# Kernel tuning notes

Hardware: AMD Instinct MI355X
Metric: run time of the kernel (lower is better)

## Reference

```python
import jax, jax.numpy as jnp
import numpy as np

BSZ, NGEN, NCLS, SEQ, G = 64, 128, 30, 2048, 16  # G = gold triples per example (fixed)

POS_NAMES = ["sub_start_logits", "sub_end_logits", "obj_start_logits", "obj_end_logits",
             "aspect_start_logits", "aspect_end_logits", "opinion_start_logits", "opinion_end_logits"]
GOLD_NAMES = ["gold_sub_start", "gold_sub_end", "gold_obj_start", "gold_obj_end",
              "gold_aspect_start", "gold_aspect_end", "gold_opinion_start", "gold_opinion_end"]


def _lsa(C):
    """Exact rectangular linear sum assignment (Jonker-Volgenant shortest augmenting
    path), equivalent to scipy.optimize.linear_sum_assignment. Returns (row_ind, col_ind)."""
    C = np.asarray(C, dtype=np.float64)
    transposed = C.shape[0] > C.shape[1]
    if transposed:
        C = C.T
    n, m = C.shape
    u = np.zeros(n + 1)
    v = np.zeros(m + 1)
    p = np.zeros(m + 1, dtype=np.int64)    # p[j] = row (1-based) assigned to column j
    way = np.zeros(m + 1, dtype=np.int64)
    for i in range(1, n + 1):
        p[0] = i
        j0 = 0
        minv = np.full(m + 1, np.inf)
        used = np.zeros(m + 1, dtype=bool)
        while True:
            used[j0] = True
            i0 = p[j0]
            cur = C[i0 - 1] - u[i0] - v[1:]
            better = (~used[1:]) & (cur < minv[1:])
            minv[1:] = np.where(better, cur, minv[1:])
            way[1:] = np.where(better, j0, way[1:])
            cand = np.where(~used[1:], minv[1:], np.inf)
            j1 = int(np.argmin(cand)) + 1
            delta = cand[j1 - 1]
            for j in np.where(used)[0]:
                u[p[j]] += delta
                v[j] -= delta
            minv[~used] -= delta
            j0 = j1
            if p[j0] == 0:
                break
        while j0:
            j1 = way[j0]
            p[j0] = p[j1]
            j0 = j1
    col = np.full(n, -1, dtype=np.int64)
    for j in range(1, m + 1):
        if p[j]:
            col[p[j] - 1] = j - 1
    row = np.arange(n, dtype=np.int64)
    if transposed:
        order = np.argsort(col)
        return col[order], row[order]
    return row, col


def setup_inputs() -> dict:
    key = jax.random.key(0)
    ks = jax.random.split(key, 18)
    d = {"pred_rel_logits": jax.random.normal(ks[0], (BSZ, NGEN, NCLS), jnp.float32)}
    for i, name in enumerate(POS_NAMES):
        d[name] = jax.random.normal(ks[1 + i], (BSZ, NGEN, SEQ), jnp.float32)
    d["gold_rel"] = jax.random.randint(ks[9], (BSZ * G,), 0, NCLS)
    for i, name in enumerate(GOLD_NAMES):
        d[name] = jax.random.randint(ks[10 + i], (BSZ * G,), 0, SEQ)
    return d


def _cost(pred_rel_logits, sub_start_logits, sub_end_logits, obj_start_logits, obj_end_logits,
          aspect_start_logits, aspect_end_logits, opinion_start_logits, opinion_end_logits,
          gold_rel, gold_sub_start, gold_sub_end, gold_obj_start, gold_obj_end,
          gold_aspect_start, gold_aspect_end, gold_opinion_start, gold_opinion_end):
    bsz, ngen = pred_rel_logits.shape[:2]
    sm = lambda x: jax.nn.softmax(x.reshape(bsz * ngen, -1), axis=-1)
    # cost: [bsz*ngen, total_gold], matcher == 'avg'
    cost = -(sm(pred_rel_logits)[:, gold_rel]
             + sm(sub_start_logits)[:, gold_sub_start] + sm(sub_end_logits)[:, gold_sub_end]
             + sm(obj_start_logits)[:, gold_obj_start] + sm(obj_end_logits)[:, gold_obj_end]
             + sm(aspect_start_logits)[:, gold_aspect_start] + sm(aspect_end_logits)[:, gold_aspect_end]
             + sm(opinion_start_logits)[:, gold_opinion_start] + sm(opinion_end_logits)[:, gold_opinion_end])
    return cost.reshape(bsz, ngen, -1)


_cost_jit = jax.jit(_cost)


def reference(pred_rel_logits, sub_start_logits, sub_end_logits, obj_start_logits, obj_end_logits,
              aspect_start_logits, aspect_end_logits, opinion_start_logits, opinion_end_logits,
              gold_rel, gold_sub_start, gold_sub_end, gold_obj_start, gold_obj_end,
              gold_aspect_start, gold_aspect_end, gold_opinion_start, gold_opinion_end):
    cost = _cost_jit(pred_rel_logits, sub_start_logits, sub_end_logits, obj_start_logits,
                     obj_end_logits, aspect_start_logits, aspect_end_logits,
                     opinion_start_logits, opinion_end_logits,
                     gold_rel, gold_sub_start, gold_sub_end, gold_obj_start, gold_obj_end,
                     gold_aspect_start, gold_aspect_end, gold_opinion_start, gold_opinion_end)
    cnp = np.asarray(cost)
    rows = np.zeros((BSZ, G), dtype=np.int64)
    cols = np.zeros((BSZ, G), dtype=np.int64)
    # per-example assignment on the example's own block of gold columns (mirrors cost.split)
    for b in range(BSZ):
        r, c = _lsa(cnp[b, :, b * G:(b + 1) * G])
        rows[b], cols[b] = r, c
    return cost, jnp.asarray(rows), jnp.asarray(cols)
```

## Files before the change

### kernel.cpp

```cpp
#include <hip/hip_runtime.h>
#include <math.h>

#define BSZ   64
#define NGEN  128
#define NCLS  30
#define SEQ   2048
#define G     16
#define NQ    (BSZ * NGEN)
#define TG    (BSZ * G)
#define COST_ELEMS ((size_t)NQ * TG)
#define OFF_ROWS COST_ELEMS
#define OFF_COLS (COST_ELEMS + TG)

__global__ __launch_bounds__(256) void cost_kernel(
    const float* __restrict__ rel,
    const float* __restrict__ p0, const float* __restrict__ p1,
    const float* __restrict__ p2, const float* __restrict__ p3,
    const float* __restrict__ p4, const float* __restrict__ p5,
    const float* __restrict__ p6, const float* __restrict__ p7,
    const int* __restrict__ grel,
    const int* __restrict__ g0, const int* __restrict__ g1,
    const int* __restrict__ g2, const int* __restrict__ g3,
    const int* __restrict__ g4, const int* __restrict__ g5,
    const int* __restrict__ g6, const int* __restrict__ g7,
    float* __restrict__ out)
{
    __shared__ float ex[4][SEQ];
    __shared__ float relex[32];

    const int q    = blockIdx.x;
    const int tid  = threadIdx.x;
    const int wave = tid >> 6;
    const int lane = tid & 63;

    float acc[4] = {0.f, 0.f, 0.f, 0.f};

    #pragma unroll
    for (int phase = 0; phase < 2; ++phase) {
        const float* pk;
        if      (wave == 0) pk = (phase == 0) ? p0 : p4;
        else if (wave == 1) pk = (phase == 0) ? p1 : p5;
        else if (wave == 2) pk = (phase == 0) ? p2 : p6;
        else                pk = (phase == 0) ? p3 : p7;

        const float4* row4 = (const float4*)(pk + (size_t)q * SEQ);
        float4 x[8];
        float mx = -INFINITY;
        #pragma unroll
        for (int j = 0; j < 8; ++j) {
            x[j] = row4[lane + 64 * j];
            mx = fmaxf(mx, fmaxf(fmaxf(x[j].x, x[j].y), fmaxf(x[j].z, x[j].w)));
        }
        #pragma unroll
        for (int off = 32; off; off >>= 1) mx = fmaxf(mx, __shfl_xor(mx, off));

        float s = 0.f;
        #pragma unroll
        for (int j = 0; j < 8; ++j) {
            x[j].x = __expf(x[j].x - mx); x[j].y = __expf(x[j].y - mx);
            x[j].z = __expf(x[j].z - mx); x[j].w = __expf(x[j].w - mx);
            s += (x[j].x + x[j].y) + (x[j].z + x[j].w);
        }
        #pragma unroll
        for (int off = 32; off; off >>= 1) s += __shfl_xor(s, off);
        const float r = 1.f / s;

        float4* exw = (float4*)ex[wave];
        #pragma unroll
        for (int j = 0; j < 8; ++j) {
            float4 e = x[j];
            e.x *= r; e.y *= r; e.z *= r; e.w *= r;
            exw[lane + 64 * j] = e;
        }

        if (phase == 0 && wave == 0) {
            float xv = (lane < NCLS) ? rel[(size_t)q * NCLS + lane] : -INFINITY;
            float m2 = xv;
            #pragma unroll
            for (int off = 32; off; off >>= 1) m2 = fmaxf(m2, __shfl_xor(m2, off));
            float e2 = (lane < NCLS) ? __expf(xv - m2) : 0.f;
            float s2 = e2;
            #pragma unroll
            for (int off = 32; off; off >>= 1) s2 += __shfl_xor(s2, off);
            float r2 = 1.f / s2;
            if (lane < 32) relex[lane] = (lane < NCLS) ? e2 * r2 : 0.f;
        }
        __syncthreads();

        const int* __restrict__ gA = phase ? g4 : g0;
        const int* __restrict__ gB = phase ? g5 : g1;
        const int* __restrict__ gC = phase ? g6 : g2;
        const int* __restrict__ gD = phase ? g7 : g3;
        #pragma unroll
        for (int c = 0; c < 4; ++c) {
            const int t = tid + 256 * c;
            acc[c] += ex[0][gA[t]];
            acc[c] += ex[1][gB[t]];
            acc[c] += ex[2][gC[t]];
            acc[c] += ex[3][gD[t]];
            if (phase == 1) acc[c] += relex[grel[t]];
        }
        __syncthreads();
    }

    #pragma unroll
    for (int c = 0; c < 4; ++c) {
        const int t = tid + 256 * c;
        out[(size_t)q * TG + t] = -acc[c];
    }
}

__global__ __launch_bounds__(64) void lsa_kernel(const float* __restrict__ cost,
                                                 float* __restrict__ out)
{
    const int b   = blockIdx.x;
    const int tid = threadIdx.x;

    __shared__ float  C[G][NGEN];
    __shared__ double u[G + 1], v[NGEN + 1], minv[NGEN + 1];
    __shared__ int    p[NGEN + 1], way[NGEN + 1], used[NGEN + 1];
    __shared__ int    colArr[G];

    for (int e = tid; e < G * NGEN; e += 64) {
        int j = e >> 4, i = e & (G - 1);
        C[i][j] = cost[((size_t)(b * NGEN + j)) * TG + b * G + i];
    }
    for (int e = tid; e <= NGEN; e += 64) { v[e] = 0.0; p[e] = 0; }
    if (tid <= G) u[tid] = 0.0;
    __syncthreads();

    const double INFD = 1e300;

    for (int i = 1; i <= G; ++i) {
        if (tid == 0) { p[0] = i; used[0] = 0; }
        #pragma unroll
        for (int c = 0; c < 2; ++c) {
            int j = 1 + tid + 64 * c;
            minv[j] = INFD; used[j] = 0;
        }
        __syncthreads();

        int j0 = 0;
        while (true) {
            if (tid == 0) used[j0] = 1;
            __syncthreads();

            const int    i0  = p[j0];
            const double ui0 = u[i0];

            double bv = INFD; int bj = NGEN + 1;
            #pragma unroll
            for (int c = 0; c < 2; ++c) {
                int j = 1 + tid + 64 * c;
                if (!used[j]) {
                    double cur = (double)C[i0 - 1][j - 1] - ui0 - v[j];
                    if (cur < minv[j]) { minv[j] = cur; way[j] = j0; }
                    double cd = minv[j];
                    if (cd < bv) { bv = cd; bj = j; }
                }
            }
            #pragma unroll
            for (int off = 32; off; off >>= 1) {
                double ov = __shfl_xor(bv, off);
                int    oj = __shfl_xor(bj, off);
                if (ov < bv || (ov == bv && oj < bj)) { bv = ov; bj = oj; }
            }
            const double delta = bv;
            const int    j1    = bj;
            __syncthreads();

            #pragma unroll
            for (int c = 0; c < 2; ++c) {
                int j = 1 + tid + 64 * c;
                if (used[j]) { u[p[j]] += delta; v[j] -= delta; }
                else         { minv[j] -= delta; }
            }
            if (tid == 0) u[p[0]] += delta;
            __syncthreads();

            j0 = j1;
            if (p[j0] == 0) break;
        }

        while (j0) {
            int j1a = way[j0];
            if (tid == 0) p[j0] = p[j1a];
            __syncthreads();
            j0 = j1a;
        }
        __syncthreads();
    }

    #pragma unroll
    for (int c = 0; c < 2; ++c) {
        int j = 1 + tid + 64 * c;
        int pi = p[j];
        if (pi != 0) colArr[pi - 1] = j - 1;
    }
    __syncthreads();
    if (tid < G) {
        int ci = colArr[tid];
        int rank = 0;
        #pragma unroll
        for (int j = 0; j < G; ++j) rank += (colArr[j] < ci) ? 1 : 0;
        out[OFF_ROWS + b * G + rank] = (float)ci;
        out[OFF_COLS + b * G + rank] = (float)tid;
    }
}

extern "C" void kernel_launch(void* const* d_in, const int* in_sizes, int n_in,
                              void* d_out, int out_size, void* d_ws, size_t ws_size,
                              hipStream_t stream) {
    const float* rel = (const float*)d_in[0];
    const float* p0  = (const float*)d_in[1];
    const float* p1  = (const float*)d_in[2];
    const float* p2  = (const float*)d_in[3];
    const float* p3  = (const float*)d_in[4];
    const float* p4  = (const float*)d_in[5];
    const float* p5  = (const float*)d_in[6];
    const float* p6  = (const float*)d_in[7];
    const float* p7  = (const float*)d_in[8];
    const int* grel = (const int*)d_in[9];
    const int* g0 = (const int*)d_in[10];
    const int* g1 = (const int*)d_in[11];
    const int* g2 = (const int*)d_in[12];
    const int* g3 = (const int*)d_in[13];
    const int* g4 = (const int*)d_in[14];
    const int* g5 = (const int*)d_in[15];
    const int* g6 = (const int*)d_in[16];
    const int* g7 = (const int*)d_in[17];
    float* out = (float*)d_out;

    cost_kernel<<<NQ, 256, 0, stream>>>(rel, p0, p1, p2, p3, p4, p5, p6, p7,
                                        grel, g0, g1, g2, g3, g4, g5, g6, g7, out);
    lsa_kernel<<<BSZ, 64, 0, stream>>>(out, out);
}
```

Before: 505.7 us.

## Widen cost blocks to 1024 threads, drop max-subtraction, register-resident single-wave LSA

The cost kernel now uses 1024 threads per query, with four waves per softmax row. It drops the max subtraction from the softmax, folds normalization into an FMA on the gather, and preloads gold indices into registers. The LSA kernel keeps u, v, minv, way, used and p in per-lane registers and communicates through wave shuffles, which removes all shared-memory barriers from the Hungarian inner loop. Skipping the max subtraction risks exp overflow on large logits. The 1024-thread blocks with 32KB of LDS may also limit occupancy.

```diff
diff --git a/kernel.cpp b/kernel.cpp
--- a/kernel.cpp
+++ b/kernel.cpp
@@ -12,7 +12,7 @@
 #define OFF_ROWS COST_ELEMS
 #define OFF_COLS (COST_ELEMS + TG)
 
-__global__ __launch_bounds__(256) void cost_kernel(
+__global__ __launch_bounds__(1024, 8) void cost_kernel(
     const float* __restrict__ rel,
     const float* __restrict__ p0, const float* __restrict__ p1,
     const float* __restrict__ p2, const float* __restrict__ p3,
@@ -27,138 +27,139 @@
 {
     __shared__ float ex[4][SEQ];
     __shared__ float relex[32];
-
+    __shared__ float spart[16];
+    __shared__ float srel;
+
+    const int tid  = threadIdx.x;
     const int q    = blockIdx.x;
-    const int tid  = threadIdx.x;
-    const int wave = tid >> 6;
     const int lane = tid & 63;
-
-    float acc[4] = {0.f, 0.f, 0.f, 0.f};
+    const int wv   = tid >> 6;
+    const int kloc = tid >> 8;
+    const int r    = tid & 255;
+
+    const int j0_ = g0[tid], j1_ = g1[tid], j2_ = g2[tid], j3_ = g3[tid];
+    const int j4_ = g4[tid], j5_ = g5[tid], j6_ = g6[tid], j7_ = g7[tid];
+    const int jr_ = grel[tid];
+
+    float acc = 0.f;
 
     #pragma unroll
     for (int phase = 0; phase < 2; ++phase) {
-        const float* pk;
-        if      (wave == 0) pk = (phase == 0) ? p0 : p4;
-        else if (wave == 1) pk = (phase == 0) ? p1 : p5;
-        else if (wave == 2) pk = (phase == 0) ? p2 : p6;
-        else                pk = (phase == 0) ? p3 : p7;
+        const float* pk =
+            (kloc == 0) ? (phase ? p4 : p0) :
+            (kloc == 1) ? (phase ? p5 : p1) :
+            (kloc == 2) ? (phase ? p6 : p2) :
+                          (phase ? p7 : p3);
 
         const float4* row4 = (const float4*)(pk + (size_t)q * SEQ);
-        float4 x[8];
-        float mx = -INFINITY;
-        #pragma unroll
-        for (int j = 0; j < 8; ++j) {
-            x[j] = row4[lane + 64 * j];
-            mx = fmaxf(mx, fmaxf(fmaxf(x[j].x, x[j].y), fmaxf(x[j].z, x[j].w)));
-        }
-        #pragma unroll
-        for (int off = 32; off; off >>= 1) mx = fmaxf(mx, __shfl_xor(mx, off));
-
-        float s = 0.f;
-        #pragma unroll
-        for (int j = 0; j < 8; ++j) {
-            x[j].x = __expf(x[j].x - mx); x[j].y = __expf(x[j].y - mx);
-            x[j].z = __expf(x[j].z - mx); x[j].w = __expf(x[j].w - mx);
-            s += (x[j].x + x[j].y) + (x[j].z + x[j].w);
-        }
+        float4 x0 = row4[r];
+        float4 x1 = row4[r + 256];
+        float4 e0, e1;
+        e0.x = __expf(x0.x); e0.y = __expf(x0.y);
+        e0.z = __expf(x0.z); e0.w = __expf(x0.w);
+        e1.x = __expf(x1.x); e1.y = __expf(x1.y);
+        e1.z = __expf(x1.z); e1.w = __expf(x1.w);
+
+        float s = ((e0.x + e0.y) + (e0.z + e0.w))
+                + ((e1.x + e1.y) + (e1.z + e1.w));
         #pragma unroll
         for (int off = 32; off; off >>= 1) s += __shfl_xor(s, off);
-        const float r = 1.f / s;
-
-        float4* exw = (float4*)ex[wave];
-        #pragma unroll
-        for (int j = 0; j < 8; ++j) {
-            float4 e = x[j];
-            e.x *= r; e.y *= r; e.z *= r; e.w *= r;
-            exw[lane + 64 * j] = e;
-        }
-
-        if (phase == 0 && wave == 0) {
-            float xv = (lane < NCLS) ? rel[(size_t)q * NCLS + lane] : -INFINITY;
-            float m2 = xv;
-            #pragma unroll
-            for (int off = 32; off; off >>= 1) m2 = fmaxf(m2, __shfl_xor(m2, off));
-            float e2 = (lane < NCLS) ? __expf(xv - m2) : 0.f;
-            float s2 = e2;
+
+        float4* exk = (float4*)ex[kloc];
+        exk[r]       = e0;
+        exk[r + 256] = e1;
+        if (lane == 0) spart[wv] = s;
+
+        if (phase == 0 && wv == 0) {
+            float e = (lane < NCLS) ? __expf(rel[(size_t)q * NCLS + lane]) : 0.f;
+            if (lane < 32) relex[lane] = e;
+            float s2 = e;
             #pragma unroll
             for (int off = 32; off; off >>= 1) s2 += __shfl_xor(s2, off);
-            float r2 = 1.f / s2;
-            if (lane < 32) relex[lane] = (lane < NCLS) ? e2 * r2 : 0.f;
+            if (lane == 0) srel = s2;
         }
         __syncthreads();
 
-        const int* __restrict__ gA = phase ? g4 : g0;
-        const int* __restrict__ gB = phase ? g5 : g1;
-        const int* __restrict__ gC = phase ? g6 : g2;
-        const int* __restrict__ gD = phase ? g7 : g3;
-        #pragma unroll
-        for (int c = 0; c < 4; ++c) {
-            const int t = tid + 256 * c;
-            acc[c] += ex[0][gA[t]];
-            acc[c] += ex[1][gB[t]];
-            acc[c] += ex[2][gC[t]];
-            acc[c] += ex[3][gD[t]];
-            if (phase == 1) acc[c] += relex[grel[t]];
-        }
-        __syncthreads();
-    }
-
-    #pragma unroll
-    for (int c = 0; c < 4; ++c) {
-        const int t = tid + 256 * c;
-        out[(size_t)q * TG + t] = -acc[c];
+        float sa = (spart[0]  + spart[1])  + (spart[2]  + spart[3]);
+        float sb = (spart[4]  + spart[5])  + (spart[6]  + spart[7]);
+        float sc = (spart[8]  + spart[9])  + (spart[10] + spart[11]);
+        float sd = (spart[12] + spart[13]) + (spart[14] + spart[15]);
+        float ra = 1.f / sa, rb = 1.f / sb, rc = 1.f / sc, rd = 1.f / sd;
+
+        if (phase == 0) {
+            acc = fmaf(ex[0][j0_], ra, acc);
+            acc = fmaf(ex[1][j1_], rb, acc);
+            acc = fmaf(ex[2][j2_], rc, acc);
+            acc = fmaf(ex[3][j3_], rd, acc);
+            __syncthreads();
+        } else {
+            acc = fmaf(ex[0][j4_], ra, acc);
+            acc = fmaf(ex[1][j5_], rb, acc);
+            acc = fmaf(ex[2][j6_], rc, acc);
+            acc = fmaf(ex[3][j7_], rd, acc);
+            acc = fmaf(relex[jr_], 1.f / srel, acc);
+            out[(size_t)q * TG + tid] = -acc;
+        }
     }
 }
 
 __global__ __launch_bounds__(64) void lsa_kernel(const float* __restrict__ cost,
                                                  float* __restrict__ out)
 {
-    const int b   = blockIdx.x;
-    const int tid = threadIdx.x;
-
-    __shared__ float  C[G][NGEN];
-    __shared__ double u[G + 1], v[NGEN + 1], minv[NGEN + 1];
-    __shared__ int    p[NGEN + 1], way[NGEN + 1], used[NGEN + 1];
-    __shared__ int    colArr[G];
-
-    for (int e = tid; e < G * NGEN; e += 64) {
+    const int b    = blockIdx.x;
+    const int lane = threadIdx.x;
+
+    __shared__ float C[G][NGEN];
+    __shared__ int   colArr[G];
+
+    for (int e = lane; e < G * NGEN; e += 64) {
         int j = e >> 4, i = e & (G - 1);
         C[i][j] = cost[((size_t)(b * NGEN + j)) * TG + b * G + i];
     }
-    for (int e = tid; e <= NGEN; e += 64) { v[e] = 0.0; p[e] = 0; }
-    if (tid <= G) u[tid] = 0.0;
     __syncthreads();
 
-    const double INFD = 1e300;
+    const double INFD = (double)INFINITY;
+
+    double u_r = 0.0;
+    double v0 = 0.0, v1 = 0.0;
+    int    p0c = 0, p1c = 0;
+    int    pcol0 = 0;
 
     for (int i = 1; i <= G; ++i) {
-        if (tid == 0) { p[0] = i; used[0] = 0; }
-        #pragma unroll
-        for (int c = 0; c < 2; ++c) {
-            int j = 1 + tid + 64 * c;
-            minv[j] = INFD; used[j] = 0;
-        }
-        __syncthreads();
-
+        pcol0 = i;
+        double minv0 = INFD, minv1 = INFD;
+        int way0 = 0, way1 = 0;
+        bool used0 = false, used1 = false;
+        bool inTree = false;
         int j0 = 0;
+
         while (true) {
-            if (tid == 0) used[j0] = 1;
-            __syncthreads();
-
-            const int    i0  = p[j0];
-            const double ui0 = u[i0];
-
-            double bv = INFD; int bj = NGEN + 1;
-            #pragma unroll
-            for (int c = 0; c < 2; ++c) {
-                int j = 1 + tid + 64 * c;
-                if (!used[j]) {
-                    double cur = (double)C[i0 - 1][j - 1] - ui0 - v[j];
-                    if (cur < minv[j]) { minv[j] = cur; way[j] = j0; }
-                    double cd = minv[j];
-                    if (cd < bv) { bv = cd; bj = j; }
-                }
-            }
+            int i0;
+            if (j0 == 0) {
+                i0 = pcol0;
+            } else {
+                int ow = (j0 - 1) & 63, c = (j0 - 1) >> 6;
+                if (lane == ow) { if (c == 0) used0 = true; else used1 = true; }
+                int pv = (c == 0) ? p0c : p1c;
+                i0 = __shfl(pv, ow);
+            }
+            if (lane == i0) inTree = true;
+            double ui0 = __shfl(u_r, i0);
+
+            float c0f = C[i0 - 1][lane];
+            float c1f = C[i0 - 1][lane + 64];
+            if (!used0) {
+                double cur = (double)c0f - ui0 - v0;
+                if (cur < minv0) { minv0 = cur; way0 = j0; }
+            }
+            if (!used1) {
+                double cur = (double)c1f - ui0 - v1;
+                if (cur < minv1) { minv1 = cur; way1 = j0; }
+            }
+
+            double bv = INFD; int bj = 1 << 30;
+            if (!used0) { bv = minv0; bj = 1 + lane; }
+            if (!used1 && minv1 < bv) { bv = minv1; bj = 65 + lane; }
             #pragma unroll
             for (int off = 32; off; off >>= 1) {
                 double ov = __shfl_xor(bv, off);
@@ -167,44 +168,44 @@
             }
             const double delta = bv;
             const int    j1    = bj;
-            __syncthreads();
-
-            #pragma unroll
-            for (int c = 0; c < 2; ++c) {
-                int j = 1 + tid + 64 * c;
-                if (used[j]) { u[p[j]] += delta; v[j] -= delta; }
-                else         { minv[j] -= delta; }
-            }
-            if (tid == 0) u[p[0]] += delta;
-            __syncthreads();
+
+            if (inTree) u_r += delta;
+            if (used0) v0 -= delta; else minv0 -= delta;
+            if (used1) v1 -= delta; else minv1 -= delta;
 
             j0 = j1;
-            if (p[j0] == 0) break;
+            int ow = (j0 - 1) & 63, c = (j0 - 1) >> 6;
+            int pv = (c == 0) ? p0c : p1c;
+            if (__shfl(pv, ow) == 0) break;
         }
 
         while (j0) {
-            int j1a = way[j0];
-            if (tid == 0) p[j0] = p[j1a];
-            __syncthreads();
-            j0 = j1a;
-        }
-        __syncthreads();
-    }
-
-    #pragma unroll
-    for (int c = 0; c < 2; ++c) {
-        int j = 1 + tid + 64 * c;
-        int pi = p[j];
-        if (pi != 0) colArr[pi - 1] = j - 1;
-    }
+            int ow = (j0 - 1) & 63, c = (j0 - 1) >> 6;
+            int wv_ = (c == 0) ? way0 : way1;
+            int j1 = __shfl(wv_, ow);
+            int pv;
+            if (j1 == 0) {
+                pv = pcol0;
+            } else {
+                int ow1 = (j1 - 1) & 63, c1 = (j1 - 1) >> 6;
+                int t2 = (c1 == 0) ? p0c : p1c;
+                pv = __shfl(t2, ow1);
+            }
+            if (lane == ow) { if (c == 0) p0c = pv; else p1c = pv; }
+            j0 = j1;
+        }
+    }
+
+    if (p0c != 0) colArr[p0c - 1] = lane;
+    if (p1c != 0) colArr[p1c - 1] = lane + 64;
     __syncthreads();
-    if (tid < G) {
-        int ci = colArr[tid];
+    if (lane < G) {
+        int ci = colArr[lane];
         int rank = 0;
         #pragma unroll
         for (int j = 0; j < G; ++j) rank += (colArr[j] < ci) ? 1 : 0;
         out[OFF_ROWS + b * G + rank] = (float)ci;
-        out[OFF_COLS + b * G + rank] = (float)tid;
+        out[OFF_COLS + b * G + rank] = (float)lane;
     }
 }
 
@@ -231,7 +232,7 @@
     const int* g7 = (const int*)d_in[17];
     float* out = (float*)d_out;
 
-    cost_kernel<<<NQ, 256, 0, stream>>>(rel, p0, p1, p2, p3, p4, p5, p6, p7,
-                                        grel, g0, g1, g2, g3, g4, g5, g6, g7, out);
+    cost_kernel<<<NQ, 1024, 0, stream>>>(rel, p0, p1, p2, p3, p4, p5, p6, p7,
+                                         grel, g0, g1, g2, g3, g4, g5, g6, g7, out);
     lsa_kernel<<<BSZ, 64, 0, stream>>>(out, out);
 }
```

After: 495.0 us. -2.1%, faster.
